# Optimization experiments

Hardware: AMD Instinct MI355X
Metric: run time of the kernel (lower is better)

Reference implementation:

```python
import jax, jax.numpy as jnp
import numpy as np

B, N, J, F, C = 8, 2048, 4, 16, 2

def setup_inputs() -> dict:
    key = jax.random.key(0)
    k1, k2, k3, k4 = jax.random.split(key, 4)
    W = jax.random.normal(k1, (B, N, N, J), dtype=jnp.float32)
    x = jax.random.normal(k2, (B, F, N, 1), dtype=jnp.float32)
    # Conv2d(F*J, C, 1) weight [C, F*J, 1, 1] -> flattened [C, F*J], plus bias [C]
    conv_w = jax.random.normal(k3, (C, F * J), dtype=jnp.float32) / np.sqrt(F * J)
    conv_b = jax.random.normal(k4, (C,), dtype=jnp.float32) * 0.01
    return {"W": W, "x": x, "conv_w": conv_w, "conv_b": conv_b}

def reference(W, x, conv_w, conv_b):
    b, n, _, j = W.shape
    f = x.shape[1]
    # gmul: out[b, j*F+f, n] = sum_m x[b,f,m] * W[b,m,n,j]
    y = jnp.einsum('bfm,bmnj->bjfn', x[..., 0], W).reshape(b, j * f, n)
    # 1x1 conv over the (J*F) channel dim
    out = jnp.einsum('ck,bkn->bcn', conv_w, y) + conv_b[None, :, None]
    # squeeze(3).transpose(1,2) -> [B, N, C] (squeeze(2) is a no-op for C=2)
    return out.transpose(0, 2, 1)
```

## Files before the change

kernel.cpp:

```cpp
#include <hip/hip_runtime.h>
#include <hip/hip_bf16.h>

constexpr int B = 8, N = 2048, J = 4, F = 16, C = 2;

typedef float fx4 __attribute__((ext_vector_type(4)));

__global__ __launch_bounds__(256) void gnn_prep_kernel(
    const float* __restrict__ x,
    const float* __restrict__ cw,
    float* __restrict__ t_ws)
{
    __shared__ float s_cw[C * J * F];
    const int tid = threadIdx.x;
    if (tid < C * J * F) s_cw[tid] = cw[tid];
    __syncthreads();

    const int gid = blockIdx.x * 256 + tid;
    const int b = gid >> 11;
    const int m = gid & (N - 1);

    const float* xb = x + (size_t)b * F * N + m;
    float xv[F];
#pragma unroll
    for (int f = 0; f < F; ++f) xv[f] = xb[(size_t)f * N];

    float t8[8];
#pragma unroll
    for (int c = 0; c < C; ++c) {
#pragma unroll
        for (int j = 0; j < J; ++j) {
            float s = 0.f;
#pragma unroll
            for (int f = 0; f < F; ++f) s += s_cw[c * (J * F) + j * F + f] * xv[f];
            t8[c * 4 + j] = s;
        }
    }
    float4* dst = (float4*)(t_ws + (size_t)gid * 8);
    dst[0] = *(float4*)&t8[0];
    dst[1] = *(float4*)&t8[4];
}

constexpr int TN = 32;
constexpr int NT = N / TN;
constexpr int BT = 512;
constexpr int MSUB = 16;
constexpr int MC = N / MSUB;

__global__ __launch_bounds__(512) void gnn_main_kernel(
    const float* __restrict__ W,
    const float* __restrict__ t_ws,
    const float* __restrict__ cb,
    float* __restrict__ out)
{
    __shared__ float tl[N * 8];
    __shared__ float red[MSUB][TN][C];

    const int tid = threadIdx.x;
    const int blk = blockIdx.x;
    const int b = blk >> 6;
    const int ntile = blk & (NT - 1);
    const int n0 = ntile * TN;

    {
        const float4* src = (const float4*)(t_ws + (size_t)b * N * 8);
        float4* dst = (float4*)tl;
#pragma unroll
        for (int i = 0; i < (N * 8 / 4) / BT; ++i)
            dst[i * BT + tid] = src[i * BT + tid];
    }
    __syncthreads();

    const int nl = tid & (TN - 1);
    const int msub = tid >> 5;
    const int m0 = msub * MC;

    const fx4* Wp = (const fx4*)W + (((size_t)b * N + m0) * N + n0 + nl);

    float acc0 = 0.f, acc1 = 0.f;
#pragma unroll 8
    for (int mi = 0; mi < MC; ++mi) {
        fx4 w4 = __builtin_nontemporal_load(Wp + (size_t)mi * N);
        const float4* tv = (const float4*)&tl[(m0 + mi) * 8];
        float4 t0 = tv[0];
        float4 t1 = tv[1];
        acc0 += w4.x * t0.x + w4.y * t0.y + w4.z * t0.z + w4.w * t0.w;
        acc1 += w4.x * t1.x + w4.y * t1.y + w4.z * t1.z + w4.w * t1.w;
    }

    red[msub][nl][0] = acc0;
    red[msub][nl][1] = acc1;
    __syncthreads();

    if (tid < TN * C) {
        const int nl2 = tid >> 1;
        const int c = tid & 1;
        float s = cb[c];
#pragma unroll
        for (int k = 0; k < MSUB; ++k) s += red[k][nl2][c];
        out[((size_t)b * N + n0 + nl2) * C + c] = s;
    }
}

extern "C" void kernel_launch(void* const* d_in, const int* in_sizes, int n_in,
                              void* d_out, int out_size, void* d_ws, size_t ws_size,
                              hipStream_t stream) {
    const float* W  = (const float*)d_in[0];
    const float* x  = (const float*)d_in[1];
    const float* cw = (const float*)d_in[2];
    const float* cb = (const float*)d_in[3];
    float* out  = (float*)d_out;
    float* t_ws = (float*)d_ws;

    gnn_prep_kernel<<<dim3(B * N / 256), dim3(256), 0, stream>>>(x, cw, t_ws);
    gnn_main_kernel<<<dim3(B * NT), dim3(BT), 0, stream>>>(W, t_ws, cb, out);
}
```

Baseline: 100.5 us.

## Split W stream over row chunks with full-width rows and separate reduce kernel

The main kernel now gives each block a chunk of 32 m-rows across all 2048 columns, so each wavefront reads whole contiguous W rows. Before, each block read a 32-column strip (512 B per row) across all rows. Each block stages only its 32 rows of t into LDS instead of the whole 64 KB per-batch table, which frees LDS and should allow more blocks per CU. Partial sums are written to a workspace of 8×64×2×2048 floats, and a third kernel adds them together with the bias. This adds a kernel launch and extra global traffic for the partials, in exchange for a more streaming access pattern over W.

```diff
diff --git a/kernel.cpp b/kernel.cpp
--- a/kernel.cpp
+++ b/kernel.cpp
@@ -2,6 +2,8 @@
 #include <hip/hip_bf16.h>
 
 constexpr int B = 8, N = 2048, J = 4, F = 16, C = 2;
+constexpr int MCH = 64;
+constexpr int MR  = N / MCH;
 
 typedef float fx4 __attribute__((ext_vector_type(4)));
 
@@ -40,65 +42,65 @@
     dst[1] = *(float4*)&t8[4];
 }
 
-constexpr int TN = 32;
-constexpr int NT = N / TN;
-constexpr int BT = 512;
-constexpr int MSUB = 16;
-constexpr int MC = N / MSUB;
-
 __global__ __launch_bounds__(512) void gnn_main_kernel(
     const float* __restrict__ W,
     const float* __restrict__ t_ws,
+    float* __restrict__ part)
+{
+    __shared__ float tl[MR * 8];
+
+    const int tid = threadIdx.x;
+    const int blk = blockIdx.x;
+    const int mc = blk & (MCH - 1);
+    const int b  = blk / MCH;
+    const int m0 = mc * MR;
+
+    if (tid < MR * 8) tl[tid] = t_ws[((size_t)b * N + m0) * 8 + tid];
+    __syncthreads();
+
+    const fx4* Wp = (const fx4*)W + ((size_t)b * N + m0) * N;
+
+    float acc[4][2] = {};
+#pragma unroll 2
+    for (int r = 0; r < MR; ++r) {
+        const fx4* row = Wp + (size_t)r * N;
+        const float4 t0 = *(const float4*)&tl[r * 8];
+        const float4 t1 = *(const float4*)&tl[r * 8 + 4];
+#pragma unroll
+        for (int k = 0; k < 4; ++k) {
+            fx4 w4 = __builtin_nontemporal_load(row + k * 512 + tid);
+            acc[k][0] += w4.x * t0.x + w4.y * t0.y + w4.z * t0.z + w4.w * t0.w;
+            acc[k][1] += w4.x * t1.x + w4.y * t1.y + w4.z * t1.z + w4.w * t1.w;
+        }
+    }
+
+    float* pb = part + (size_t)blk * C * N;
+#pragma unroll
+    for (int k = 0; k < 4; ++k) {
+        const int n = k * 512 + tid;
+        pb[n]     = acc[k][0];
+        pb[N + n] = acc[k][1];
+    }
+}
+
+__global__ __launch_bounds__(256) void gnn_reduce_kernel(
+    const float* __restrict__ part,
     const float* __restrict__ cb,
     float* __restrict__ out)
 {
-    __shared__ float tl[N * 8];
-    __shared__ float red[MSUB][TN][C];
+    const int gid = blockIdx.x * 256 + threadIdx.x;
+    const int b = gid >> 11;
+    const int n = gid & (N - 1);
 
-    const int tid = threadIdx.x;
-    const int blk = blockIdx.x;
-    const int b = blk >> 6;
-    const int ntile = blk & (NT - 1);
-    const int n0 = ntile * TN;
-
-    {
-        const float4* src = (const float4*)(t_ws + (size_t)b * N * 8);
-        float4* dst = (float4*)tl;
-#pragma unroll
-        for (int i = 0; i < (N * 8 / 4) / BT; ++i)
-            dst[i * BT + tid] = src[i * BT + tid];
+    float s0 = cb[0], s1 = cb[1];
+    const float* pb = part + (size_t)b * MCH * C * N + n;
+#pragma unroll 8
+    for (int mcc = 0; mcc < MCH; ++mcc) {
+        s0 += pb[(size_t)(mcc * C + 0) * N];
+        s1 += pb[(size_t)(mcc * C + 1) * N];
     }
-    __syncthreads();
-
-    const int nl = tid & (TN - 1);
-    const int msub = tid >> 5;
-    const int m0 = msub * MC;
-
-    const fx4* Wp = (const fx4*)W + (((size_t)b * N + m0) * N + n0 + nl);
-
-    float acc0 = 0.f, acc1 = 0.f;
-#pragma unroll 8
-    for (int mi = 0; mi < MC; ++mi) {
-        fx4 w4 = __builtin_nontemporal_load(Wp + (size_t)mi * N);
-        const float4* tv = (const float4*)&tl[(m0 + mi) * 8];
-        float4 t0 = tv[0];
-        float4 t1 = tv[1];
-        acc0 += w4.x * t0.x + w4.y * t0.y + w4.z * t0.z + w4.w * t0.w;
-        acc1 += w4.x * t1.x + w4.y * t1.y + w4.z * t1.z + w4.w * t1.w;
-    }
-
-    red[msub][nl][0] = acc0;
-    red[msub][nl][1] = acc1;
-    __syncthreads();
-
-    if (tid < TN * C) {
-        const int nl2 = tid >> 1;
-        const int c = tid & 1;
-        float s = cb[c];
-#pragma unroll
-        for (int k = 0; k < MSUB; ++k) s += red[k][nl2][c];
-        out[((size_t)b * N + n0 + nl2) * C + c] = s;
-    }
+    float2 o; o.x = s0; o.y = s1;
+    *(float2*)&out[(size_t)gid * C] = o;
 }
 
 extern "C" void kernel_launch(void* const* d_in, const int* in_sizes, int n_in,
@@ -110,7 +112,9 @@
     const float* cb = (const float*)d_in[3];
     float* out  = (float*)d_out;
     float* t_ws = (float*)d_ws;
+    float* part = t_ws + (size_t)B * N * 8;
 
     gnn_prep_kernel<<<dim3(B * N / 256), dim3(256), 0, stream>>>(x, cw, t_ws);
-    gnn_main_kernel<<<dim3(B * NT), dim3(BT), 0, stream>>>(W, t_ws, cb, out);
+    gnn_main_kernel<<<dim3(B * MCH), dim3(512), 0, stream>>>(W, t_ws, part);
+    gnn_reduce_kernel<<<dim3(B * N / 256), dim3(256), 0, stream>>>(part, cb, out);
 }
```

Result: faster. 97.95 us (-2.5%).
